# Kernel tuning notes

Hardware: AMD Instinct MI355X
Metric: run time of the kernel (lower is better)

Reference implementation:

```python
import jax, jax.numpy as jnp
import numpy as np

B, D, H = 4096, 2048, 2048

def setup_inputs() -> dict:
    key = jax.random.key(0)
    ks = jax.random.split(key, 16)
    s = 0.02  # small scale to keep tanh/sigmoid out of saturation
    inp = {
        'input_': jax.random.normal(ks[0], (B, D), jnp.float32),
        'h_prev': jax.random.normal(ks[1], (B, H), jnp.float32),
        'c_prev': jax.random.normal(ks[2], (B, H), jnp.float32),
        'w_xi': jax.random.normal(ks[3], (D, H), jnp.float32) * s,
        'w_hi': jax.random.normal(ks[4], (H, H), jnp.float32) * s,
        'w_ci': jax.random.normal(ks[5], (H, H), jnp.float32) * s,
        'w_xf': jax.random.normal(ks[6], (D, H), jnp.float32) * s,
        'w_hf': jax.random.normal(ks[7], (H, H), jnp.float32) * s,
        'w_cf': jax.random.normal(ks[8], (H, H), jnp.float32) * s,
        'w_xg': jax.random.normal(ks[9], (D, H), jnp.float32) * s,
        'w_hg': jax.random.normal(ks[10], (H, H), jnp.float32) * s,
        'w_xo': jax.random.normal(ks[11], (D, H), jnp.float32) * s,
        'w_ho': jax.random.normal(ks[12], (H, H), jnp.float32) * s,
        'w_co': jax.random.normal(ks[13], (H, H), jnp.float32) * s,
        'w_c':  jax.random.normal(ks[14], (H, H), jnp.float32) * s,
        'w_i':  jax.random.normal(ks[15], (D, H), jnp.float32) * s,
        'b_i': jnp.zeros((H,), jnp.float32),
        'b_f': jnp.zeros((H,), jnp.float32),
        'b_g': jnp.zeros((H,), jnp.float32),
        'b_o': jnp.zeros((H,), jnp.float32),
    }
    return inp

def reference(input_, h_prev, c_prev,
              w_xi, w_hi, w_ci, w_xf, w_hf, w_cf, w_xg, w_hg,
              w_xo, w_ho, w_co, w_c, w_i,
              b_i, b_f, b_g, b_o):
    # Fuse the x- and h-path GEMMs into concatenated matmuls (math-identical).
    wx = jnp.concatenate([w_xi, w_xf, w_xg, w_xo, w_i], axis=1)   # [D, 5H]
    wh = jnp.concatenate([w_hi, w_hf, w_hg, w_ho], axis=1)        # [H, 4H]
    wc = jnp.concatenate([w_ci, w_cf], axis=1)                    # [H, 2H]
    xz = input_ @ wx                                              # [B, 5H]
    hz = h_prev @ wh                                              # [B, 4H]
    cz = c_prev @ wc                                              # [B, 2H]
    Hd = w_hi.shape[0]
    i = xz[:, 0*Hd:1*Hd] + hz[:, 0*Hd:1*Hd] + cz[:, 0*Hd:1*Hd] + b_i
    f = xz[:, 1*Hd:2*Hd] + hz[:, 1*Hd:2*Hd] + cz[:, 1*Hd:2*Hd] + b_f
    g = xz[:, 2*Hd:3*Hd] + hz[:, 2*Hd:3*Hd] + b_g
    c = jax.nn.sigmoid(f) * c_prev + jax.nn.sigmoid(i) * jnp.tanh(g)
    o = xz[:, 3*Hd:4*Hd] + hz[:, 3*Hd:4*Hd] + c @ w_co + b_o
    h = jnp.tanh(o) * (jnp.tanh(c) @ w_c + xz[:, 4*Hd:5*Hd])
    return (h, c)
```

## Files before the change

### kernel.cpp

```cpp
#include <hip/hip_runtime.h>
#include <cstdint>
#include <cstddef>

typedef unsigned short u16;
typedef __bf16 bf16x8 __attribute__((ext_vector_type(8)));
typedef float f32x4 __attribute__((ext_vector_type(4)));
typedef u16 u16x8 __attribute__((ext_vector_type(8)));

#define B_DIM 4096
#define H_DIM 2048
#define BH 8388608

__device__ __forceinline__ float b2f(u16 x) {
  union { uint32_t u; float f; } v;
  v.u = ((uint32_t)x) << 16;
  return v.f;
}
__device__ __forceinline__ u16 f2b(float f) {
  union { float f; uint32_t u; } v;
  v.f = f;
  uint32_t r = v.u + 0x7FFFu + ((v.u >> 16) & 1u);
  return (u16)(r >> 16);
}
__device__ __forceinline__ float sigm(float x) { return 1.0f / (1.0f + __expf(-x)); }

typedef __attribute__((address_space(1))) void gv_t;
typedef __attribute__((address_space(3))) void lv_t;
__device__ __forceinline__ void g2lds16(const void* g, void* l) {
  __builtin_amdgcn_global_load_lds((gv_t*)g, (lv_t*)l, 16, 0, 0);
}

struct CvtParams { const float* src[3]; u16* dst[3]; };

__global__ __launch_bounds__(256) void cvt_k(CvtParams p) {
  const float* __restrict__ s = p.src[blockIdx.y];
  u16* __restrict__ d = p.dst[blockIdx.y];
  size_t idx = ((size_t)blockIdx.x * 256 + threadIdx.x) * 8;
  float4 a = *(const float4*)(s + idx);
  float4 b = *(const float4*)(s + idx + 4);
  u16x8 o;
  o[0] = f2b(a.x); o[1] = f2b(a.y); o[2] = f2b(a.z); o[3] = f2b(a.w);
  o[4] = f2b(b.x); o[5] = f2b(b.y); o[6] = f2b(b.z); o[7] = f2b(b.w);
  *(u16x8*)(d + idx) = o;
}

struct TransParams {
  const float* src[13];
  u16* dst[13];
  int dstride[13];
};

__global__ __launch_bounds__(256) void transpose_k(TransParams p) {
  __shared__ u16 lds[64][72];
  const int mat = blockIdx.z;
  const float* __restrict__ src = p.src[mat];
  u16* __restrict__ dst = p.dst[mat];
  const int dstride = p.dstride[mat];
  const int tk = blockIdx.y * 64;
  const int tn = blockIdx.x * 64;
  const int t = threadIdx.x;
  const int lr = t >> 3;
  const int lc = (t & 7) * 8;
#pragma unroll
  for (int half = 0; half < 2; half++) {
    int r = lr + half * 32;
    const float4* g = (const float4*)(src + (size_t)(tk + r) * 2048 + tn + lc);
    float4 a = g[0], b = g[1];
    u16x8 t8;
    t8[0] = f2b(a.x); t8[1] = f2b(a.y); t8[2] = f2b(a.z); t8[3] = f2b(a.w);
    t8[4] = f2b(b.x); t8[5] = f2b(b.y); t8[6] = f2b(b.z); t8[7] = f2b(b.w);
    *(u16x8*)&lds[r][lc] = t8;
  }
  __syncthreads();
#pragma unroll
  for (int half = 0; half < 2; half++) {
    int n = lr + half * 32;
    u16x8 tmp;
#pragma unroll
    for (int j = 0; j < 8; j++) tmp[j] = lds[lc + j][n];
    *(u16x8*)(dst + (size_t)(tn + n) * dstride + tk + lc) = tmp;
  }
}

__device__ __forceinline__ void seg2048(
    const u16* __restrict__ Aseg,
    const u16* __restrict__ Wseg,
    long ldW,
    u16* ldsA, u16* ldsB,
    int wave, int lane,
    int wm, int wn, int fm, int fkc,
    f32x4 (&acc)[4][4]) {
  const int sr8 = lane >> 3;
  const int slot = lane & 7;
  const int sc = ((slot ^ sr8) << 3);
  const u16* pA[4]; const u16* pB[4];
  u16* lA[4]; u16* lB[4];
#pragma unroll
  for (int i = 0; i < 4; i++) {
    int rl = wave * 32 + i * 8;
    pA[i] = Aseg + (size_t)(rl + sr8) * 2048 + sc;
    pB[i] = Wseg + (size_t)(rl + sr8) * ldW + sc;
    lA[i] = ldsA + rl * 64;
    lB[i] = ldsB + rl * 64;
  }
  const int x7 = fm & 7;
  int raBase[4], rbBase[4];
#pragma unroll
  for (int i = 0; i < 4; i++) {
    raBase[i] = (wm + i * 16 + fm) * 64;
    rbBase[i] = (wn + i * 16 + fm) * 64;
  }
  for (int it = 0; it < 32; ++it) {
    __syncthreads();
#pragma unroll
    for (int i = 0; i < 4; i++) { g2lds16(pA[i], lA[i]); g2lds16(pB[i], lB[i]); }
    __syncthreads();
#pragma unroll
    for (int ks = 0; ks < 2; ks++) {
      const int c = ks * 4 + fkc;
      const int so = ((c ^ x7) << 3);
      bf16x8 af[4], bfr[4];
#pragma unroll
      for (int i = 0; i < 4; i++) {
        af[i] = *(const bf16x8*)&ldsA[raBase[i] + so];
        bfr[i] = *(const bf16x8*)&ldsB[rbBase[i] + so];
      }
#pragma unroll
      for (int i = 0; i < 4; i++)
#pragma unroll
        for (int j = 0; j < 4; j++)
          acc[i][j] = __builtin_amdgcn_mfma_f32_16x16x32_bf16(af[i], bfr[j], acc[i][j], 0, 0, 0);
    }
#pragma unroll
    for (int i = 0; i < 4; i++) { pA[i] += 64; pB[i] += 64; }
  }
}

struct GemmDesc {
  const u16* A0; const u16* A1; const u16* A2;
  const u16* Wt; u16* C; int nseg;
};
struct GemmParams { GemmDesc d[5]; };

__global__ __launch_bounds__(256) void gemm_multi(GemmParams p) {
  const GemmDesc d = p.d[blockIdx.z];
  const int nseg = d.nseg;
  const long Ktot = (long)nseg * 2048;

  __shared__ u16 ldsA[128 * 64];
  __shared__ u16 ldsB[128 * 64];

  const int t = threadIdx.x;
  const int wave = t >> 6, lane = t & 63;
  const int m0 = blockIdx.y * 128, n0 = blockIdx.x * 128;
  const int fm = lane & 15, fkc = lane >> 4;
  const int wm = (wave >> 1) * 64, wn = (wave & 1) * 64;

  f32x4 acc[4][4];
#pragma unroll
  for (int i = 0; i < 4; i++)
#pragma unroll
    for (int j = 0; j < 4; j++) acc[i][j] = (f32x4)0.0f;

  for (int seg = 0; seg < nseg; ++seg) {
    const u16* As = (seg == 0) ? d.A0 : ((seg == 1) ? d.A1 : d.A2);
    seg2048(As + (size_t)m0 * 2048,
            d.Wt + (size_t)n0 * Ktot + (size_t)seg * 2048, Ktot,
            ldsA, ldsB, wave, lane, wm, wn, fm, fkc, acc);
  }

  const int quad = lane >> 4;
#pragma unroll
  for (int i = 0; i < 4; i++) {
#pragma unroll
    for (int j = 0; j < 4; j++) {
#pragma unroll
      for (int r = 0; r < 4; r++) {
        size_t row = (size_t)(m0 + wm + i * 16 + quad * 4 + r);
        size_t col = (size_t)(n0 + wn + j * 16 + fm);
        d.C[row * 2048 + col] = f2b(acc[i][j][r]);
      }
    }
  }
}

__global__ __launch_bounds__(256) void gemm_res(
    const u16* __restrict__ cb16, const u16* __restrict__ tcb16,
    const u16* __restrict__ WtCO, const u16* __restrict__ WtC,
    const u16* __restrict__ zo, const u16* __restrict__ zr,
    const float* __restrict__ bo, float* __restrict__ h_out) {
  __shared__ u16 ldsA[128 * 64];
  __shared__ u16 ldsB[128 * 64];

  const int t = threadIdx.x;
  const int wave = t >> 6, lane = t & 63;
  const int m0 = blockIdx.y * 128, n0 = blockIdx.x * 128;
  const int fm = lane & 15, fkc = lane >> 4;
  const int wm = (wave >> 1) * 64, wn = (wave & 1) * 64;

  f32x4 acc[4][4];
#pragma unroll
  for (int i = 0; i < 4; i++)
#pragma unroll
    for (int j = 0; j < 4; j++) acc[i][j] = (f32x4)0.0f;

  seg2048(cb16 + (size_t)m0 * 2048, WtCO + (size_t)n0 * 2048, 2048,
          ldsA, ldsB, wave, lane, wm, wn, fm, fkc, acc);

  uint32_t t1p[4][4][2];
#pragma unroll
  for (int i = 0; i < 4; i++)
#pragma unroll
    for (int j = 0; j < 4; j++)
#pragma unroll
      for (int pp = 0; pp < 2; pp++)
        t1p[i][j][pp] = (uint32_t)f2b(acc[i][j][2 * pp]) |
                        ((uint32_t)f2b(acc[i][j][2 * pp + 1]) << 16);

#pragma unroll
  for (int i = 0; i < 4; i++)
#pragma unroll
    for (int j = 0; j < 4; j++) acc[i][j] = (f32x4)0.0f;

  seg2048(tcb16 + (size_t)m0 * 2048, WtC + (size_t)n0 * 2048, 2048,
          ldsA, ldsB, wave, lane, wm, wn, fm, fkc, acc);

  const int quad = lane >> 4;
#pragma unroll
  for (int i = 0; i < 4; i++) {
#pragma unroll
    for (int j = 0; j < 4; j++) {
      int col = n0 + wn + j * 16 + fm;
      float bov = bo[col];
#pragma unroll
      for (int r = 0; r < 4; r++) {
        size_t row = (size_t)(m0 + wm + i * 16 + quad * 4 + r);
        size_t idx = row * 2048 + (size_t)col;
        float t1 = b2f((u16)(t1p[i][j][r >> 1] >> ((r & 1) * 16)));
        float ov = b2f(zo[idx]) + t1 + bov;
        float hv = tanhf(ov) * (b2f(zr[idx]) + acc[i][j][r]);
        h_out[idx] = hv;
      }
    }
  }
}

__global__ __launch_bounds__(256) void ew1_k(
    u16* __restrict__ zi, const u16* __restrict__ zf, u16* __restrict__ zg,
    const float* __restrict__ cprev, const float* __restrict__ bi,
    const float* __restrict__ bff, const float* __restrict__ bg,
    float* __restrict__ c_out) {
  size_t idx = ((size_t)blockIdx.x * 256 + threadIdx.x) * 8;
  int col = (int)(idx & (H_DIM - 1));
  u16x8 vzi = *(const u16x8*)(zi + idx);
  u16x8 vzf = *(const u16x8*)(zf + idx);
  u16x8 vzg = *(const u16x8*)(zg + idx);
  float4 cp0 = *(const float4*)(cprev + idx);
  float4 cp1 = *(const float4*)(cprev + idx + 4);
  float4 bi0 = *(const float4*)(bi + col), bi1 = *(const float4*)(bi + col + 4);
  float4 bf0 = *(const float4*)(bff + col), bf1 = *(const float4*)(bff + col + 4);
  float4 bg0 = *(const float4*)(bg + col), bg1 = *(const float4*)(bg + col + 4);
  float cpv[8] = {cp0.x, cp0.y, cp0.z, cp0.w, cp1.x, cp1.y, cp1.z, cp1.w};
  float biv[8] = {bi0.x, bi0.y, bi0.z, bi0.w, bi1.x, bi1.y, bi1.z, bi1.w};
  float bfv[8] = {bf0.x, bf0.y, bf0.z, bf0.w, bf1.x, bf1.y, bf1.z, bf1.w};
  float bgv[8] = {bg0.x, bg0.y, bg0.z, bg0.w, bg1.x, bg1.y, bg1.z, bg1.w};
  float cv[8], tcv[8];
#pragma unroll
  for (int e = 0; e < 8; e++) {
    float iv = b2f(vzi[e]) + biv[e];
    float fv = b2f(vzf[e]) + bfv[e];
    float gv = b2f(vzg[e]) + bgv[e];
    float c = sigm(fv) * cpv[e] + sigm(iv) * tanhf(gv);
    cv[e] = c;
    tcv[e] = tanhf(c);
  }
  u16x8 cb8, tc8;
#pragma unroll
  for (int e = 0; e < 8; e++) { cb8[e] = f2b(cv[e]); tc8[e] = f2b(tcv[e]); }
  *(u16x8*)(zi + idx) = cb8;
  *(u16x8*)(zg + idx) = tc8;
  float4 c0 = {cv[0], cv[1], cv[2], cv[3]}, c1 = {cv[4], cv[5], cv[6], cv[7]};
  *(float4*)(c_out + idx) = c0;
  *(float4*)(c_out + idx + 4) = c1;
}

extern "C" void kernel_launch(void* const* d_in, const int* in_sizes, int n_in,
                              void* d_out, int out_size, void* d_ws, size_t ws_size,
                              hipStream_t stream) {
  const float* input_ = (const float*)d_in[0];
  const float* h_prev = (const float*)d_in[1];
  const float* c_prev = (const float*)d_in[2];
  const float* w_xi = (const float*)d_in[3];
  const float* w_hi = (const float*)d_in[4];
  const float* w_ci = (const float*)d_in[5];
  const float* w_xf = (const float*)d_in[6];
  const float* w_hf = (const float*)d_in[7];
  const float* w_cf = (const float*)d_in[8];
  const float* w_xg = (const float*)d_in[9];
  const float* w_hg = (const float*)d_in[10];
  const float* w_xo = (const float*)d_in[11];
  const float* w_ho = (const float*)d_in[12];
  const float* w_co = (const float*)d_in[13];
  const float* w_c  = (const float*)d_in[14];
  const float* w_i  = (const float*)d_in[15];
  const float* b_i  = (const float*)d_in[16];
  const float* b_f  = (const float*)d_in[17];
  const float* b_g  = (const float*)d_in[18];
  const float* b_o  = (const float*)d_in[19];

  u16* ws = (u16*)d_ws;
  u16* WtI  = ws;
  u16* WtF  = WtI  + (size_t)2048 * 6144;
  u16* WtG  = WtF  + (size_t)2048 * 6144;
  u16* WtO  = WtG  + (size_t)2048 * 4096;
  u16* WtR  = WtO  + (size_t)2048 * 4096;
  u16* WtCO = WtR  + (size_t)2048 * 2048;
  u16* WtC  = WtCO + (size_t)2048 * 2048;
  u16* zi   = WtC  + (size_t)2048 * 2048;
  u16* zf   = zi + (size_t)BH;
  u16* zg   = zf + (size_t)BH;
  u16* zo   = zg + (size_t)BH;
  u16* zr   = zo + (size_t)BH;

  u16* ob16 = (u16*)d_out;
  u16* xb = ob16;
  u16* hb = ob16 + (size_t)BH;
  u16* cb = ob16 + (size_t)2 * BH;
  float* out_f = (float*)d_out;
  float* h_out = out_f;
  float* c_out = out_f + (size_t)BH;

  CvtParams cp;
  cp.src[0] = input_; cp.src[1] = h_prev; cp.src[2] = c_prev;
  cp.dst[0] = xb; cp.dst[1] = hb; cp.dst[2] = cb;
  cvt_k<<<dim3(BH / 2048, 3), 256, 0, stream>>>(cp);

  TransParams tp;
  const float* srcs[13] = {w_xi, w_hi, w_ci, w_xf, w_hf, w_cf, w_xg, w_hg, w_xo, w_ho, w_i, w_co, w_c};
  u16* dsts[13] = {WtI, WtI + 2048, WtI + 4096, WtF, WtF + 2048, WtF + 4096,
                   WtG, WtG + 2048, WtO, WtO + 2048, WtR, WtCO, WtC};
  int strides[13] = {6144, 6144, 6144, 6144, 6144, 6144, 4096, 4096, 4096, 4096, 2048, 2048, 2048};
  for (int i = 0; i < 13; i++) { tp.src[i] = srcs[i]; tp.dst[i] = dsts[i]; tp.dstride[i] = strides[i]; }
  transpose_k<<<dim3(32, 32, 13), 256, 0, stream>>>(tp);

  GemmParams g1;
  g1.d[0] = {xb, hb, cb, WtI, zi, 3};
  g1.d[1] = {xb, hb, cb, WtF, zf, 3};
  g1.d[2] = {xb, hb, nullptr, WtG, zg, 2};
  g1.d[3] = {xb, hb, nullptr, WtO, zo, 2};
  g1.d[4] = {xb, nullptr, nullptr, WtR, zr, 1};
  gemm_multi<<<dim3(16, 32, 5), 256, 0, stream>>>(g1);

  ew1_k<<<dim3(BH / 2048), 256, 0, stream>>>(zi, zf, zg, c_prev, b_i, b_f, b_g, c_out);

  gemm_res<<<dim3(16, 32), 256, 0, stream>>>(zi, zg, WtCO, WtC, zo, zr, b_o, h_out);
}
```

Measured before the change: 890.9 us.

## Use 256x256 double-buffered MFMA GEMM tiles and split residual GEMMs

Replaces the 128x128 single-buffered GEMM tile loop with a 256x256 tile, 512-thread kernel. It double-buffers A and B in LDS with interleaved global-to-LDS prefetch, uses barrier-scheduled MFMA phases with priority hints, and swizzles block order for L2 reuse. The two residual GEMMs (c@w_co and tanh(c)@w_c) now run as independent z-slices of one launch, writing intermediates to reused workspace, and a new elementwise kernel computes h from them. This aims to raise arithmetic intensity and hide load latency, at the cost of an extra kernel and extra intermediate memory traffic.

```diff
diff --git a/kernel.cpp b/kernel.cpp
--- a/kernel.cpp
+++ b/kernel.cpp
@@ -29,6 +29,8 @@
 __device__ __forceinline__ void g2lds16(const void* g, void* l) {
   __builtin_amdgcn_global_load_lds((gv_t*)g, (lv_t*)l, 16, 0, 0);
 }
+
+#define MFMA_BF16 __builtin_amdgcn_mfma_f32_16x16x32_bf16
 
 struct CvtParams { const float* src[3]; u16* dst[3]; };
 
@@ -82,166 +84,219 @@
   }
 }
 
-__device__ __forceinline__ void seg2048(
-    const u16* __restrict__ Aseg,
-    const u16* __restrict__ Wseg,
-    long ldW,
-    u16* ldsA, u16* ldsB,
-    int wave, int lane,
-    int wm, int wn, int fm, int fkc,
-    f32x4 (&acc)[4][4]) {
-  const int sr8 = lane >> 3;
-  const int slot = lane & 7;
-  const int sc = ((slot ^ sr8) << 3);
-  const u16* pA[4]; const u16* pB[4];
-  u16* lA[4]; u16* lB[4];
-#pragma unroll
-  for (int i = 0; i < 4; i++) {
-    int rl = wave * 32 + i * 8;
-    pA[i] = Aseg + (size_t)(rl + sr8) * 2048 + sc;
-    pB[i] = Wseg + (size_t)(rl + sr8) * ldW + sc;
-    lA[i] = ldsA + rl * 64;
-    lB[i] = ldsB + rl * 64;
-  }
+__device__ __forceinline__ void kloop256(
+    const u16* __restrict__ A0, const u16* __restrict__ A1, const u16* __restrict__ A2,
+    const u16* __restrict__ Wt, const int NT, const long Ktot,
+    const int m0, const int n0,
+    u16* lA0, u16* lA1, u16* lB0, u16* lB1,
+    f32x4 (&acc)[8][4]) {
+  const int tid = threadIdx.x;
+  const int wave = tid >> 6, lane = tid & 63;
+  const int fm = lane & 15, fkc = lane >> 4;
   const int x7 = fm & 7;
-  int raBase[4], rbBase[4];
-#pragma unroll
-  for (int i = 0; i < 4; i++) {
-    raBase[i] = (wm + i * 16 + fm) * 64;
-    rbBase[i] = (wn + i * 16 + fm) * 64;
-  }
-  for (int it = 0; it < 32; ++it) {
-    __syncthreads();
-#pragma unroll
-    for (int i = 0; i < 4; i++) { g2lds16(pA[i], lA[i]); g2lds16(pB[i], lB[i]); }
-    __syncthreads();
-#pragma unroll
-    for (int ks = 0; ks < 2; ks++) {
-      const int c = ks * 4 + fkc;
-      const int so = ((c ^ x7) << 3);
-      bf16x8 af[4], bfr[4];
-#pragma unroll
-      for (int i = 0; i < 4; i++) {
-        af[i] = *(const bf16x8*)&ldsA[raBase[i] + so];
-        bfr[i] = *(const bf16x8*)&ldsB[rbBase[i] + so];
-      }
-#pragma unroll
-      for (int i = 0; i < 4; i++)
-#pragma unroll
-        for (int j = 0; j < 4; j++)
-          acc[i][j] = __builtin_amdgcn_mfma_f32_16x16x32_bf16(af[i], bfr[j], acc[i][j], 0, 0, 0);
+  const int wm = (wave >> 2) * 128, wn = (wave & 3) * 64;
+  const int lr = tid >> 3;
+  const int chunk = (tid & 7) ^ (lr & 7);
+  const int stageOff = wave * 512;
+
+  int raOff[8], rbOff[4];
+#pragma unroll
+  for (int i = 0; i < 8; i++) raOff[i] = (wm + i * 16 + fm) * 64;
+#pragma unroll
+  for (int j = 0; j < 4; j++) rbOff[j] = (wn + j * 16 + fm) * 64;
+  const int so0 = ((fkc ^ x7) << 3);
+  const int so1 = (((4 + fkc) ^ x7) << 3);
+
+  auto stA = [&](int tt, int a, u16* dst) {
+    const int seg = tt >> 5;
+    const u16* base = (seg == 0) ? A0 : ((seg == 1) ? A1 : A2);
+    const u16* src = base + (size_t)(m0 + a * 64 + lr) * 2048 + ((tt & 31) << 6) + (chunk << 3);
+    g2lds16(src, dst + a * 4096 + stageOff);
+  };
+  auto stB = [&](int tt, int b, u16* dst) {
+    const u16* src = Wt + (size_t)(n0 + b * 64 + lr) * Ktot + ((size_t)tt << 6) + (chunk << 3);
+    g2lds16(src, dst + b * 4096 + stageOff);
+  };
+
+#pragma unroll
+  for (int a = 0; a < 4; a++) stA(0, a, lA0);
+#pragma unroll
+  for (int b = 0; b < 4; b++) stB(0, b, lB0);
+  const int t1p = (1 < NT) ? 1 : 0;
+#pragma unroll
+  for (int a = 0; a < 4; a++) stA(t1p, a, lA1);
+  asm volatile("s_waitcnt vmcnt(4)" ::: "memory");
+  __builtin_amdgcn_sched_barrier(0);
+  __builtin_amdgcn_s_barrier();
+  __builtin_amdgcn_sched_barrier(0);
+
+  for (int t = 0; t < NT; ++t) {
+    u16* lAp = (t & 1) ? lA1 : lA0;
+    u16* lBp = (t & 1) ? lB1 : lB0;
+    u16* lBq = (t & 1) ? lB0 : lB1;
+    const int tn1 = (t + 1 < NT) ? t + 1 : NT - 1;
+    const int tn2 = (t + 2 < NT) ? t + 2 : NT - 1;
+
+    bf16x8 a0[8], b0[4];
+#pragma unroll
+    for (int i = 0; i < 8; i++) a0[i] = *(const bf16x8*)&lAp[raOff[i] + so0];
+#pragma unroll
+    for (int j = 0; j < 4; j++) b0[j] = *(const bf16x8*)&lBp[rbOff[j] + so0];
+    stB(tn1, 0, lBq);
+    stB(tn1, 1, lBq);
+    __builtin_amdgcn_s_barrier();
+    asm volatile("s_waitcnt lgkmcnt(0)" ::: "memory");
+    __builtin_amdgcn_sched_barrier(0);
+    __builtin_amdgcn_s_setprio(1);
+#pragma unroll
+    for (int i = 0; i < 8; i++) {
+      acc[i][0] = MFMA_BF16(a0[i], b0[0], acc[i][0], 0, 0, 0);
+      acc[i][1] = MFMA_BF16(a0[i], b0[1], acc[i][1], 0, 0, 0);
     }
-#pragma unroll
-    for (int i = 0; i < 4; i++) { pA[i] += 64; pB[i] += 64; }
-  }
-}
-
-struct GemmDesc {
+    __builtin_amdgcn_s_setprio(0);
+    __builtin_amdgcn_sched_barrier(0);
+    __builtin_amdgcn_s_barrier();
+    __builtin_amdgcn_sched_barrier(0);
+
+    stB(tn1, 2, lBq);
+    stB(tn1, 3, lBq);
+    __builtin_amdgcn_s_barrier();
+    __builtin_amdgcn_sched_barrier(0);
+    __builtin_amdgcn_s_setprio(1);
+#pragma unroll
+    for (int i = 0; i < 8; i++) {
+      acc[i][2] = MFMA_BF16(a0[i], b0[2], acc[i][2], 0, 0, 0);
+      acc[i][3] = MFMA_BF16(a0[i], b0[3], acc[i][3], 0, 0, 0);
+    }
+    __builtin_amdgcn_s_setprio(0);
+    __builtin_amdgcn_sched_barrier(0);
+    __builtin_amdgcn_s_barrier();
+    __builtin_amdgcn_sched_barrier(0);
+
+    bf16x8 a1[8], b1[4];
+#pragma unroll
+    for (int i = 0; i < 8; i++) a1[i] = *(const bf16x8*)&lAp[raOff[i] + so1];
+#pragma unroll
+    for (int j = 0; j < 4; j++) b1[j] = *(const bf16x8*)&lBp[rbOff[j] + so1];
+    __builtin_amdgcn_s_barrier();
+    asm volatile("s_waitcnt lgkmcnt(0)" ::: "memory");
+    __builtin_amdgcn_sched_barrier(0);
+    __builtin_amdgcn_s_setprio(1);
+#pragma unroll
+    for (int i = 0; i < 8; i++) {
+      acc[i][0] = MFMA_BF16(a1[i], b1[0], acc[i][0], 0, 0, 0);
+      acc[i][1] = MFMA_BF16(a1[i], b1[1], acc[i][1], 0, 0, 0);
+    }
+    __builtin_amdgcn_s_setprio(0);
+    __builtin_amdgcn_sched_barrier(0);
+    __builtin_amdgcn_s_barrier();
+    __builtin_amdgcn_sched_barrier(0);
+
+    stA(tn2, 0, lAp);
+    stA(tn2, 1, lAp);
+    stA(tn2, 2, lAp);
+    stA(tn2, 3, lAp);
+    __builtin_amdgcn_s_barrier();
+    __builtin_amdgcn_sched_barrier(0);
+    __builtin_amdgcn_s_setprio(1);
+#pragma unroll
+    for (int i = 0; i < 8; i++) {
+      acc[i][2] = MFMA_BF16(a1[i], b1[2], acc[i][2], 0, 0, 0);
+      acc[i][3] = MFMA_BF16(a1[i], b1[3], acc[i][3], 0, 0, 0);
+    }
+    __builtin_amdgcn_s_setprio(0);
+    asm volatile("s_waitcnt vmcnt(4)" ::: "memory");
+    __builtin_amdgcn_sched_barrier(0);
+    __builtin_amdgcn_s_barrier();
+    __builtin_amdgcn_sched_barrier(0);
+  }
+}
+
+struct Gemm256Desc {
   const u16* A0; const u16* A1; const u16* A2;
   const u16* Wt; u16* C; int nseg;
 };
-struct GemmParams { GemmDesc d[5]; };
-
-__global__ __launch_bounds__(256) void gemm_multi(GemmParams p) {
-  const GemmDesc d = p.d[blockIdx.z];
-  const int nseg = d.nseg;
-  const long Ktot = (long)nseg * 2048;
-
-  __shared__ u16 ldsA[128 * 64];
-  __shared__ u16 ldsB[128 * 64];
-
-  const int t = threadIdx.x;
-  const int wave = t >> 6, lane = t & 63;
-  const int m0 = blockIdx.y * 128, n0 = blockIdx.x * 128;
-  const int fm = lane & 15, fkc = lane >> 4;
-  const int wm = (wave >> 1) * 64, wn = (wave & 1) * 64;
-
-  f32x4 acc[4][4];
-#pragma unroll
-  for (int i = 0; i < 4; i++)
+struct Gemm256Params { Gemm256Desc d[5]; };
+
+__global__ __launch_bounds__(512) void gemm256_multi(Gemm256Params p) {
+  const Gemm256Desc d = p.d[blockIdx.z];
+  __shared__ u16 lA[2][16384];
+  __shared__ u16 lB[2][16384];
+  const int bid = blockIdx.y * 8 + blockIdx.x;
+  const int swz = (bid & 7) * 16 + (bid >> 3);
+  const int m0 = (swz >> 3) * 256, n0 = (swz & 7) * 256;
+  const int NT = d.nseg << 5;
+  const long Ktot = (long)NT << 6;
+
+  f32x4 acc[8][4];
+#pragma unroll
+  for (int i = 0; i < 8; i++)
 #pragma unroll
     for (int j = 0; j < 4; j++) acc[i][j] = (f32x4)0.0f;
 
-  for (int seg = 0; seg < nseg; ++seg) {
-    const u16* As = (seg == 0) ? d.A0 : ((seg == 1) ? d.A1 : d.A2);
-    seg2048(As + (size_t)m0 * 2048,
-            d.Wt + (size_t)n0 * Ktot + (size_t)seg * 2048, Ktot,
-            ldsA, ldsB, wave, lane, wm, wn, fm, fkc, acc);
-  }
-
-  const int quad = lane >> 4;
-#pragma unroll
-  for (int i = 0; i < 4; i++) {
-#pragma unroll
-    for (int j = 0; j < 4; j++) {
+  kloop256(d.A0, d.A1, d.A2, d.Wt, NT, Ktot, m0, n0, lA[0], lA[1], lB[0], lB[1], acc);
+
+  const int lane = threadIdx.x & 63, wave = threadIdx.x >> 6;
+  const int fm = lane & 15, quad = lane >> 4;
+  const int wm = (wave >> 2) * 128, wn = (wave & 3) * 64;
+#pragma unroll
+  for (int i = 0; i < 8; i++)
+#pragma unroll
+    for (int j = 0; j < 4; j++)
 #pragma unroll
       for (int r = 0; r < 4; r++) {
         size_t row = (size_t)(m0 + wm + i * 16 + quad * 4 + r);
         size_t col = (size_t)(n0 + wn + j * 16 + fm);
         d.C[row * 2048 + col] = f2b(acc[i][j][r]);
       }
-    }
-  }
-}
-
-__global__ __launch_bounds__(256) void gemm_res(
-    const u16* __restrict__ cb16, const u16* __restrict__ tcb16,
-    const u16* __restrict__ WtCO, const u16* __restrict__ WtC,
-    const u16* __restrict__ zo, const u16* __restrict__ zr,
-    const float* __restrict__ bo, float* __restrict__ h_out) {
-  __shared__ u16 ldsA[128 * 64];
-  __shared__ u16 ldsB[128 * 64];
-
-  const int t = threadIdx.x;
-  const int wave = t >> 6, lane = t & 63;
-  const int m0 = blockIdx.y * 128, n0 = blockIdx.x * 128;
-  const int fm = lane & 15, fkc = lane >> 4;
-  const int wm = (wave >> 1) * 64, wn = (wave & 1) * 64;
-
-  f32x4 acc[4][4];
-#pragma unroll
-  for (int i = 0; i < 4; i++)
+}
+
+struct GemmResParams {
+  const u16* A[2]; const u16* W[2];
+  u16* t1; float* t2;
+};
+
+__global__ __launch_bounds__(512) void gemm256_res(GemmResParams p) {
+  const int z = blockIdx.z;
+  __shared__ u16 lA[2][16384];
+  __shared__ u16 lB[2][16384];
+  const int bid = blockIdx.y * 8 + blockIdx.x;
+  const int swz = (bid & 7) * 16 + (bid >> 3);
+  const int m0 = (swz >> 3) * 256, n0 = (swz & 7) * 256;
+
+  f32x4 acc[8][4];
+#pragma unroll
+  for (int i = 0; i < 8; i++)
 #pragma unroll
     for (int j = 0; j < 4; j++) acc[i][j] = (f32x4)0.0f;
 
-  seg2048(cb16 + (size_t)m0 * 2048, WtCO + (size_t)n0 * 2048, 2048,
-          ldsA, ldsB, wave, lane, wm, wn, fm, fkc, acc);
-
-  uint32_t t1p[4][4][2];
-#pragma unroll
-  for (int i = 0; i < 4; i++)
-#pragma unroll
-    for (int j = 0; j < 4; j++)
-#pragma unroll
-      for (int pp = 0; pp < 2; pp++)
-        t1p[i][j][pp] = (uint32_t)f2b(acc[i][j][2 * pp]) |
-                        ((uint32_t)f2b(acc[i][j][2 * pp + 1]) << 16);
-
-#pragma unroll
-  for (int i = 0; i < 4; i++)
-#pragma unroll
-    for (int j = 0; j < 4; j++) acc[i][j] = (f32x4)0.0f;
-
-  seg2048(tcb16 + (size_t)m0 * 2048, WtC + (size_t)n0 * 2048, 2048,
-          ldsA, ldsB, wave, lane, wm, wn, fm, fkc, acc);
-
-  const int quad = lane >> 4;
-#pragma unroll
-  for (int i = 0; i < 4; i++) {
-#pragma unroll
-    for (int j = 0; j < 4; j++) {
-      int col = n0 + wn + j * 16 + fm;
-      float bov = bo[col];
-#pragma unroll
-      for (int r = 0; r < 4; r++) {
-        size_t row = (size_t)(m0 + wm + i * 16 + quad * 4 + r);
-        size_t idx = row * 2048 + (size_t)col;
-        float t1 = b2f((u16)(t1p[i][j][r >> 1] >> ((r & 1) * 16)));
-        float ov = b2f(zo[idx]) + t1 + bov;
-        float hv = tanhf(ov) * (b2f(zr[idx]) + acc[i][j][r]);
-        h_out[idx] = hv;
-      }
-    }
+  kloop256(p.A[z], nullptr, nullptr, p.W[z], 32, 2048, m0, n0, lA[0], lA[1], lB[0], lB[1], acc);
+
+  const int lane = threadIdx.x & 63, wave = threadIdx.x >> 6;
+  const int fm = lane & 15, quad = lane >> 4;
+  const int wm = (wave >> 2) * 128, wn = (wave & 3) * 64;
+  if (z == 0) {
+#pragma unroll
+    for (int i = 0; i < 8; i++)
+#pragma unroll
+      for (int j = 0; j < 4; j++)
+#pragma unroll
+        for (int r = 0; r < 4; r++) {
+          size_t row = (size_t)(m0 + wm + i * 16 + quad * 4 + r);
+          size_t col = (size_t)(n0 + wn + j * 16 + fm);
+          p.t1[row * 2048 + col] = f2b(acc[i][j][r]);
+        }
+  } else {
+#pragma unroll
+    for (int i = 0; i < 8; i++)
+#pragma unroll
+      for (int j = 0; j < 4; j++)
+#pragma unroll
+        for (int r = 0; r < 4; r++) {
+          size_t row = (size_t)(m0 + wm + i * 16 + quad * 4 + r);
+          size_t col = (size_t)(n0 + wn + j * 16 + fm);
+          p.t2[row * 2048 + col] = acc[i][j][r];
+        }
   }
 }
 
@@ -282,6 +337,32 @@
   float4 c0 = {cv[0], cv[1], cv[2], cv[3]}, c1 = {cv[4], cv[5], cv[6], cv[7]};
   *(float4*)(c_out + idx) = c0;
   *(float4*)(c_out + idx + 4) = c1;
+}
+
+__global__ __launch_bounds__(256) void ew2_k(
+    const u16* __restrict__ zo, const u16* __restrict__ zr,
+    const u16* __restrict__ t1, const float* __restrict__ t2,
+    const float* __restrict__ bo, float* __restrict__ h) {
+  size_t idx = ((size_t)blockIdx.x * 256 + threadIdx.x) * 8;
+  int col = (int)(idx & (H_DIM - 1));
+  u16x8 vo = *(const u16x8*)(zo + idx);
+  u16x8 vr = *(const u16x8*)(zr + idx);
+  u16x8 v1 = *(const u16x8*)(t1 + idx);
+  float4 t2a = *(const float4*)(t2 + idx);
+  float4 t2b = *(const float4*)(t2 + idx + 4);
+  float4 bo0 = *(const float4*)(bo + col);
+  float4 bo1 = *(const float4*)(bo + col + 4);
+  float t2v[8] = {t2a.x, t2a.y, t2a.z, t2a.w, t2b.x, t2b.y, t2b.z, t2b.w};
+  float bov[8] = {bo0.x, bo0.y, bo0.z, bo0.w, bo1.x, bo1.y, bo1.z, bo1.w};
+  float hv[8];
+#pragma unroll
+  for (int e = 0; e < 8; e++) {
+    float ov = b2f(vo[e]) + b2f(v1[e]) + bov[e];
+    hv[e] = tanhf(ov) * (b2f(vr[e]) + t2v[e]);
+  }
+  float4 h0 = {hv[0], hv[1], hv[2], hv[3]}, h1 = {hv[4], hv[5], hv[6], hv[7]};
+  *(float4*)(h + idx) = h0;
+  *(float4*)(h + idx + 4) = h1;
 }
 
 extern "C" void kernel_launch(void* const* d_in, const int* in_sizes, int n_in,
@@ -322,6 +403,9 @@
   u16* zo   = zg + (size_t)BH;
   u16* zr   = zo + (size_t)BH;
 
+  u16* t1buf = WtG;
+  float* t2buf = (float*)WtI;
+
   u16* ob16 = (u16*)d_out;
   u16* xb = ob16;
   u16* hb = ob16 + (size_t)BH;
@@ -343,15 +427,20 @@
   for (int i = 0; i < 13; i++) { tp.src[i] = srcs[i]; tp.dst[i] = dsts[i]; tp.dstride[i] = strides[i]; }
   transpose_k<<<dim3(32, 32, 13), 256, 0, stream>>>(tp);
 
-  GemmParams g1;
+  Gemm256Params g1;
   g1.d[0] = {xb, hb, cb, WtI, zi, 3};
   g1.d[1] = {xb, hb, cb, WtF, zf, 3};
   g1.d[2] = {xb, hb, nullptr, WtG, zg, 2};
   g1.d[3] = {xb, hb, nullptr, WtO, zo, 2};
   g1.d[4] = {xb, nullptr, nullptr, WtR, zr, 1};
-  gemm_multi<<<dim3(16, 32, 5), 256, 0, stream>>>(g1);
+  gemm256_multi<<<dim3(8, 16, 5), 512, 0, stream>>>(g1);
 
   ew1_k<<<dim3(BH / 2048), 256, 0, stream>>>(zi, zf, zg, c_prev, b_i, b_f, b_g, c_out);
 
-  gemm_res<<<dim3(16, 32), 256, 0, stream>>>(zi, zg, WtCO, WtC, zo, zr, b_o, h_out);
-}
+  GemmResParams gr;
+  gr.A[0] = zi; gr.A[1] = zg; gr.W[0] = WtCO; gr.W[1] = WtC;
+  gr.t1 = t1buf; gr.t2 = t2buf;
+  gemm256_res<<<dim3(8, 16, 2), 512, 0, stream>>>(gr);
+
+  ew2_k<<<dim3(BH / 2048), 256, 0, stream>>>(zo, zr, t1buf, t2buf, b_o, h_out);
+}
```

Measured after the change: 804.5 us. 1.11x faster.
